# Kernel tuning notes

Measured on AMD Instinct MI355X. Metric: run time of the kernel, lower is better.

Reference implementation:

```python
import jax, jax.numpy as jnp
import numpy as np

# Whisper-small decoder, prefill path (text_offset == 0, no KV caches)
L, D, H, V, NCTX, S_AUDIO, B, T, MAXC = 12, 768, 12, 51865, 448, 1500, 2, 192, 256
DH = D // H
SCALE = DH ** -0.5
EPS = 1e-5

PNAMES = ['attn_ln_g', 'attn_ln_b', 'attn_q_w', 'attn_q_b', 'attn_k_w', 'attn_v_w', 'attn_v_b',
          'attn_o_w', 'attn_o_b', 'cross_ln_g', 'cross_ln_b', 'cross_q_w', 'cross_q_b',
          'cross_k_w', 'cross_v_w', 'cross_v_b', 'cross_o_w', 'cross_o_b',
          'mlp_ln_g', 'mlp_ln_b', 'mlp_w1', 'mlp_b1', 'mlp_w2', 'mlp_b2', 'ln_g', 'ln_b']


def _ln(x, g, b):
    m = jnp.mean(x, -1, keepdims=True)
    v = jnp.mean((x - m) ** 2, -1, keepdims=True)
    return (x - m) * jax.lax.rsqrt(v + EPS) * g + b


def _heads(t):
    b, t_, _ = t.shape
    return t.reshape(b, t_, H, DH).transpose(0, 2, 1, 3)  # (b,H,t,DH)


def _mha(q, k, v, mask):
    qh, kh, vh = _heads(q), _heads(k), _heads(v)
    qk = jnp.matmul(qh, kh.swapaxes(-1, -2)) * SCALE  # (B,H,Tq,Tk), broadcasts over kv batch 1
    if mask is not None:
        qk = qk + mask
    w = jax.nn.softmax(qk, axis=-1)
    o = jnp.matmul(w, vh)  # (B,H,Tq,DH)
    o = o.transpose(0, 2, 1, 3).reshape(q.shape[0], q.shape[1], D)
    return o, qk


def _lin(x, w, b=None):
    y = jnp.einsum('bti,oi->bto', x, w)
    return y if b is None else y + b


def _forward(x, xa, tok_emb, pos_emb, P):
    h = tok_emb[x] + pos_emb[:T]                        # (B,T,D)
    h = jnp.pad(h, ((0, 0), (0, MAXC - T), (0, 0)))     # pad to max_n_ctx_for_1st=256
    r = jnp.arange(MAXC)
    mask = jnp.where((r[None, :] > r[:, None]) | (r[None, :] >= T), -jnp.inf, 0.0)
    xa1 = xa[:1]                                        # xa.split(1)[0] in torch
    cross_qks, new_mkv, new_ckv = [], [], []
    for l in range(L):
        y = _ln(h, P['attn_ln_g'][l], P['attn_ln_b'][l])
        q = _lin(y, P['attn_q_w'][l], P['attn_q_b'][l])
        k = _lin(y, P['attn_k_w'][l])
        v = _lin(y, P['attn_v_w'][l], P['attn_v_b'][l])
        new_mkv += [k, v]
        o, _ = _mha(q, k, v, mask)
        h = h + _lin(o, P['attn_o_w'][l], P['attn_o_b'][l])
        y = _ln(h, P['cross_ln_g'][l], P['cross_ln_b'][l])
        q = _lin(y, P['cross_q_w'][l], P['cross_q_b'][l])
        ck = _lin(xa1, P['cross_k_w'][l])
        cv = _lin(xa1, P['cross_v_w'][l], P['cross_v_b'][l])
        new_ckv += [ck, cv]
        o, cqk = _mha(q, ck, cv, None)
        cross_qks.append(jax.lax.stop_gradient(cqk))    # qk.detach() in torch
        h = h + _lin(o, P['cross_o_w'][l], P['cross_o_b'][l])
        y = _ln(h, P['mlp_ln_g'][l], P['mlp_ln_b'][l])
        h = h + _lin(jax.nn.gelu(_lin(y, P['mlp_w1'][l], P['mlp_b1'][l]), approximate=False),
                     P['mlp_w2'][l], P['mlp_b2'][l])
    h = _ln(h, P['ln_g'], P['ln_b'])
    logits = jnp.matmul(h[:, :T], tok_emb.T).astype(jnp.float32)       # (B,T,V)
    cross_qks = jnp.concatenate(cross_qks, axis=0)[:, :, :T, :]        # (L*B,H,T,S_AUDIO)
    return logits, cross_qks, jnp.stack(new_mkv), jnp.stack(new_ckv)


def setup_inputs() -> dict:
    key = jax.random.key(0)
    ks = iter(jax.random.split(key, 48))
    def p(shape, s=0.02):
        return jax.random.normal(next(ks), shape, jnp.float32) * s
    inp = {
        'x': jax.random.randint(next(ks), (B, T), 0, V, dtype=jnp.int32),
        'xa': jax.random.normal(next(ks), (B, S_AUDIO, D), jnp.float32),
        'text_offset': 0,
        'isNewCKV': 1,
        'tok_emb': p((V, D)),
        'pos_emb': p((NCTX, D)),
        'attn_ln_g': 1.0 + p((L, D)), 'attn_ln_b': p((L, D)),
        'attn_q_w': p((L, D, D)), 'attn_q_b': p((L, D)),
        'attn_k_w': p((L, D, D)),
        'attn_v_w': p((L, D, D)), 'attn_v_b': p((L, D)),
        'attn_o_w': p((L, D, D)), 'attn_o_b': p((L, D)),
        'cross_ln_g': 1.0 + p((L, D)), 'cross_ln_b': p((L, D)),
        'cross_q_w': p((L, D, D)), 'cross_q_b': p((L, D)),
        'cross_k_w': p((L, D, D)),
        'cross_v_w': p((L, D, D)), 'cross_v_b': p((L, D)),
        'cross_o_w': p((L, D, D)), 'cross_o_b': p((L, D)),
        'mlp_ln_g': 1.0 + p((L, D)), 'mlp_ln_b': p((L, D)),
        'mlp_w1': p((L, 4 * D, D)), 'mlp_b1': p((L, 4 * D)),
        'mlp_w2': p((L, D, 4 * D)), 'mlp_b2': p((L, D)),
        'ln_g': 1.0 + p((D,)), 'ln_b': p((D,)),
    }
    return inp


def reference(x, xa, text_offset, isNewCKV, tok_emb, pos_emb,
              attn_ln_g, attn_ln_b, attn_q_w, attn_q_b, attn_k_w, attn_v_w, attn_v_b,
              attn_o_w, attn_o_b, cross_ln_g, cross_ln_b, cross_q_w, cross_q_b,
              cross_k_w, cross_v_w, cross_v_b, cross_o_w, cross_o_b,
              mlp_ln_g, mlp_ln_b, mlp_w1, mlp_b1, mlp_w2, mlp_b2, ln_g, ln_b):
    # text_offset == 0 prefill path; isNewCKV unused in the pure-python torch path
    P = dict(zip(PNAMES, (attn_ln_g, attn_ln_b, attn_q_w, attn_q_b, attn_k_w, attn_v_w, attn_v_b,
                          attn_o_w, attn_o_b, cross_ln_g, cross_ln_b, cross_q_w, cross_q_b,
                          cross_k_w, cross_v_w, cross_v_b, cross_o_w, cross_o_b,
                          mlp_ln_g, mlp_ln_b, mlp_w1, mlp_b1, mlp_w2, mlp_b2, ln_g, ln_b)))
    return _forward(x, xa, tok_emb, pos_emb, P)
```

## Files before the change

kernel.cpp:

```cpp
#include <hip/hip_runtime.h>
#include <math.h>

constexpr int kL = 12, kD = 768, kH = 12, kV = 51865, kSA = 1500;
constexpr int kB = 2, kT = 192, kMC = 256, kDH = 64;
constexpr float kScale = 0.125f;
constexpr float kEps = 1e-5f;
constexpr int kR = kB * kMC;
constexpr int kSLDc = 1504;

constexpr size_t SZ_LOGITS = (size_t)kB * kT * kV;
constexpr size_t SZ_CQK    = (size_t)kL * kB * kH * kT * kSA;
constexpr size_t SZ_MKV    = (size_t)2 * kL * kB * kMC * kD;
constexpr size_t OFF_CQK = SZ_LOGITS;
constexpr size_t OFF_MKV = OFF_CQK + SZ_CQK;
constexpr size_t OFF_CKV = OFF_MKV + SZ_MKV;

typedef float f32x4v __attribute__((ext_vector_type(4)));
typedef unsigned short us8v __attribute__((ext_vector_type(8)));
typedef unsigned short us4v __attribute__((ext_vector_type(4)));
typedef unsigned int   u32x4 __attribute__((ext_vector_type(4)));

static __device__ __forceinline__ unsigned short f2bf(float f) {
    unsigned int u = __float_as_uint(f);
    u += 0x7fffu + ((u >> 16) & 1u);
    return (unsigned short)(u >> 16);
}

static __device__ __forceinline__ unsigned int f2bf2(float lo, float hi) {
    unsigned int r;
    asm("v_cvt_pk_bf16_f32 %0, %1, %2" : "=v"(r) : "v"(lo), "v"(hi));
    return r;
}

static __device__ __forceinline__ float bf2f(unsigned short u) {
    return __uint_as_float((unsigned int)u << 16);
}

static __device__ __forceinline__ f32x4v mfma_bf16(us8v a, us8v b, f32x4v c) {
    asm("v_mfma_f32_16x16x32_bf16 %0, %1, %2, %0" : "+v"(c) : "v"(a), "v"(b));
    return c;
}

__global__ void k_embed(const int* __restrict__ x, const float* __restrict__ tok,
                        const float* __restrict__ pos, float* __restrict__ h)
{
    int idx = blockIdx.x * 256 + threadIdx.x;
    int d = idx % kD;
    int t = (idx / kD) % kMC;
    int b = idx / (kD * kMC);
    float v = 0.f;
    if (t < kT) {
        int tokid = x[b * kT + t];
        v = tok[(size_t)tokid * kD + d] + pos[(size_t)t * kD + d];
    }
    h[idx] = v;
}

__global__ void k_ln(const float* __restrict__ in, const float* __restrict__ g,
                     const float* __restrict__ bb, unsigned short* __restrict__ out)
{
    int r = blockIdx.x;
    const float* xr = in + (size_t)r * kD;
    int t = threadIdx.x;
    float x0 = xr[t], x1 = xr[t + 256], x2 = xr[t + 512];
    float s  = x0 + x1 + x2;
    float sq = x0 * x0 + x1 * x1 + x2 * x2;
    __shared__ float red[8];
    for (int o = 32; o > 0; o >>= 1) { s += __shfl_down(s, o); sq += __shfl_down(sq, o); }
    int w = t >> 6;
    if ((t & 63) == 0) { red[w] = s; red[4 + w] = sq; }
    __syncthreads();
    s  = red[0] + red[1] + red[2] + red[3];
    sq = red[4] + red[5] + red[6] + red[7];
    float m   = s * (1.f / kD);
    float var = sq * (1.f / kD) - m * m;
    float rs  = rsqrtf(var + kEps);
    unsigned short* orow = out + (size_t)r * kD;
    orow[t]       = f2bf((x0 - m) * rs * g[t]       + bb[t]);
    orow[t + 256] = f2bf((x1 - m) * rs * g[t + 256] + bb[t + 256]);
    orow[t + 512] = f2bf((x2 - m) * rs * g[t + 512] + bb[t + 512]);
}

__global__ void k_finalln(const float* __restrict__ h, const float* __restrict__ g,
                          const float* __restrict__ bb, unsigned short* __restrict__ out)
{
    int r = blockIdx.x;
    int b = r / kT, tt = r % kT;
    const float* xr = h + (size_t)(b * kMC + tt) * kD;
    int t = threadIdx.x;
    float x0 = xr[t], x1 = xr[t + 256], x2 = xr[t + 512];
    float s  = x0 + x1 + x2;
    float sq = x0 * x0 + x1 * x1 + x2 * x2;
    __shared__ float red[8];
    for (int o = 32; o > 0; o >>= 1) { s += __shfl_down(s, o); sq += __shfl_down(sq, o); }
    int w = t >> 6;
    if ((t & 63) == 0) { red[w] = s; red[4 + w] = sq; }
    __syncthreads();
    s  = red[0] + red[1] + red[2] + red[3];
    sq = red[4] + red[5] + red[6] + red[7];
    float m   = s * (1.f / kD);
    float var = sq * (1.f / kD) - m * m;
    float rs  = rsqrtf(var + kEps);
    unsigned short* orow = out + (size_t)r * kD;
    orow[t]       = f2bf((x0 - m) * rs * g[t]       + bb[t]);
    orow[t + 256] = f2bf((x1 - m) * rs * g[t + 256] + bb[t + 256]);
    orow[t + 512] = f2bf((x2 - m) * rs * g[t + 512] + bb[t + 512]);
}

struct GEntry { const float* W; const float* bias; const float* res; void* out; };
struct GBatch { GEntry e[24]; };

template <int ABF, int OBF>
__global__ __launch_bounds__(256)
void gemm_t(const void* __restrict__ Av, GBatch gb, int M, int N, int K,
            int dogelu)
{
    constexpr int LD = 72;
    __shared__ unsigned short As[3][64][LD];
    __shared__ unsigned short Ws[3][64][LD];
    const GEntry ge = gb.e[blockIdx.z];
    const float* __restrict__ W = ge.W;
    int bn = blockIdx.y * 64;
    int bm = blockIdx.x * 64;
    int tid = threadIdx.x;
    int wid = tid >> 6, lane = tid & 63;
    int wm = (wid >> 1) * 32, wn = (wid & 1) * 32;
    int l15 = lane & 15, lg = lane >> 4;
    int r = tid >> 2, cq = (tid & 3) * 16;
    int gr = bm + r, gc = bn + r;

    auto load_a = [&](int k0, u32x4& p0, u32x4& p1) {
        p0 = (u32x4){}; p1 = (u32x4){};
        if (ABF) {
            if (gr < M) {
                const unsigned short* ar =
                    (const unsigned short*)Av + (size_t)gr * K + k0 + cq;
                p0 = *(const u32x4*)ar;
                p1 = *(const u32x4*)(ar + 8);
            }
        } else {
            if (gr < M) {
                const float* ar = (const float*)Av + (size_t)gr * K + k0 + cq;
                float4 v0 = *(const float4*)(ar);
                float4 v1 = *(const float4*)(ar + 4);
                float4 v2 = *(const float4*)(ar + 8);
                float4 v3 = *(const float4*)(ar + 12);
                p0[0] = f2bf2(v0.x, v0.y); p0[1] = f2bf2(v0.z, v0.w);
                p0[2] = f2bf2(v1.x, v1.y); p0[3] = f2bf2(v1.z, v1.w);
                p1[0] = f2bf2(v2.x, v2.y); p1[1] = f2bf2(v2.z, v2.w);
                p1[2] = f2bf2(v3.x, v3.y); p1[3] = f2bf2(v3.z, v3.w);
            }
        }
    };
    auto load_w = [&](int k0, u32x4& p0, u32x4& p1) {
        p0 = (u32x4){}; p1 = (u32x4){};
        if (gc < N) {
            const float* wr = W + (size_t)gc * K + k0 + cq;
            float4 v0 = *(const float4*)(wr);
            float4 v1 = *(const float4*)(wr + 4);
            float4 v2 = *(const float4*)(wr + 8);
            float4 v3 = *(const float4*)(wr + 12);
            p0[0] = f2bf2(v0.x, v0.y); p0[1] = f2bf2(v0.z, v0.w);
            p0[2] = f2bf2(v1.x, v1.y); p0[3] = f2bf2(v1.z, v1.w);
            p1[0] = f2bf2(v2.x, v2.y); p1[1] = f2bf2(v2.z, v2.w);
            p1[2] = f2bf2(v3.x, v3.y); p1[3] = f2bf2(v3.z, v3.w);
        }
    };
    auto stage = [&](int buf, u32x4 a0, u32x4 a1, u32x4 w0, u32x4 w1) {
        *(u32x4*)&As[buf][r][cq]     = a0;
        *(u32x4*)&As[buf][r][cq + 8] = a1;
        *(u32x4*)&Ws[buf][r][cq]     = w0;
        *(u32x4*)&Ws[buf][r][cq + 8] = w1;
    };

    f32x4v acc00 = {}, acc01 = {}, acc10 = {}, acc11 = {};
    auto domfma = [&](int buf) {
        #pragma unroll
        for (int kc = 0; kc < 2; ++kc) {
            us8v af0 = *(const us8v*)&As[buf][wm + l15][kc * 32 + lg * 8];
            us8v af1 = *(const us8v*)&As[buf][wm + 16 + l15][kc * 32 + lg * 8];
            us8v wf0 = *(const us8v*)&Ws[buf][wn + l15][kc * 32 + lg * 8];
            us8v wf1 = *(const us8v*)&Ws[buf][wn + 16 + l15][kc * 32 + lg * 8];
            acc00 = mfma_bf16(af0, wf0, acc00);
            acc01 = mfma_bf16(af0, wf1, acc01);
            acc10 = mfma_bf16(af1, wf0, acc10);
            acc11 = mfma_bf16(af1, wf1, acc11);
        }
    };

    u32x4 a0A, a1A, w0A, w1A, a0B, a1B, w0B, w1B;
    load_a(0, a0A, a1A); load_w(0, w0A, w1A);
    stage(0, a0A, a1A, w0A, w1A);
    load_a(64, a0B, a1B); load_w(64, w0B, w1B);
    __syncthreads();

    int cur = 0;
    for (int k0 = 0; k0 < K; k0 += 128) {
        int n1 = cur + 1; if (n1 == 3) n1 = 0;
        int n2 = n1 + 1; if (n2 == 3) n2 = 0;
        if (k0 + 128 < K) { load_a(k0 + 128, a0A, a1A); load_w(k0 + 128, w0A, w1A); }
        domfma(cur);
        stage(n1, a0B, a1B, w0B, w1B);
        __syncthreads();
        if (k0 + 192 < K) { load_a(k0 + 192, a0B, a1B); load_w(k0 + 192, w0B, w1B); }
        domfma(n1);
        if (k0 + 128 < K) {
            stage(n2, a0A, a1A, w0A, w1A);
            __syncthreads();
        }
        cur = n2;
    }

    const float* bias = ge.bias;
    const float* res  = ge.res;
    f32x4v accs[2][2] = { { acc00, acc01 }, { acc10, acc11 } };
    #pragma unroll
    for (int fi = 0; fi < 2; ++fi) {
        #pragma unroll
        for (int fj = 0; fj < 2; ++fj) {
            int col = bn + wn + fj * 16 + l15;
            if (col >= N) continue;
            float bv = bias ? bias[col] : 0.f;
            #pragma unroll
            for (int rr = 0; rr < 4; ++rr) {
                int row = bm + wm + fi * 16 + lg * 4 + rr;
                if (row >= M) continue;
                float v = accs[fi][fj][rr] + bv;
                if (dogelu) v = 0.5f * v * (1.f + erff(v * 0.70710678118654752f));
                if (OBF) {
                    ((unsigned short*)ge.out)[(size_t)row * N + col] = f2bf(v);
                } else {
                    if (res) v += res[(size_t)row * N + col];
                    ((float*)ge.out)[(size_t)row * N + col] = v;
                }
            }
        }
    }
}

template <int OBF>
__global__ __launch_bounds__(256)
void gemm32(const unsigned short* __restrict__ A, GBatch gb, int M, int N, int K,
            int dogelu)
{
    constexpr int LD = 72;
    __shared__ unsigned short As[3][32][LD];
    __shared__ unsigned short Ws[3][64][LD];
    const GEntry ge = gb.e[blockIdx.z];
    const float* __restrict__ W = ge.W;
    int bn = blockIdx.y * 64;
    int bm = blockIdx.x * 32;
    int tid = threadIdx.x;
    int wid = tid >> 6, lane = tid & 63;
    int wr = (wid >> 1) * 16, wc = (wid & 1) * 32;
    int l15 = lane & 15, lg = lane >> 4;
    int ra = tid >> 3, ca = (tid & 7) * 8;
    int rw = tid >> 2, cw = (tid & 3) * 16;
    int gr = bm + ra, gc = bn + rw;

    auto load_a = [&](int k0, us8v& p) {
        p = (us8v){};
        if (gr < M) p = *(const us8v*)(A + (size_t)gr * K + k0 + ca);
    };
    auto load_w = [&](int k0, u32x4& p0, u32x4& p1) {
        p0 = (u32x4){}; p1 = (u32x4){};
        if (gc < N) {
            const float* wrp = W + (size_t)gc * K + k0 + cw;
            float4 v0 = *(const float4*)(wrp);
            float4 v1 = *(const float4*)(wrp + 4);
            float4 v2 = *(const float4*)(wrp + 8);
            float4 v3 = *(const float4*)(wrp + 12);
            p0[0] = f2bf2(v0.x, v0.y); p0[1] = f2bf2(v0.z, v0.w);
            p0[2] = f2bf2(v1.x, v1.y); p0[3] = f2bf2(v1.z, v1.w);
            p1[0] = f2bf2(v2.x, v2.y); p1[1] = f2bf2(v2.z, v2.w);
            p1[2] = f2bf2(v3.x, v3.y); p1[3] = f2bf2(v3.z, v3.w);
        }
    };
    auto stage = [&](int buf, us8v a, u32x4 w0, u32x4 w1) {
        *(us8v*)&As[buf][ra][ca]      = a;
        *(u32x4*)&Ws[buf][rw][cw]     = w0;
        *(u32x4*)&Ws[buf][rw][cw + 8] = w1;
    };

    f32x4v acc0 = {}, acc1 = {};
    auto domfma = [&](int buf) {
        #pragma unroll
        for (int kc = 0; kc < 2; ++kc) {
            us8v af  = *(const us8v*)&As[buf][wr + l15][kc * 32 + lg * 8];
            us8v wf0 = *(const us8v*)&Ws[buf][wc + l15][kc * 32 + lg * 8];
            us8v wf1 = *(const us8v*)&Ws[buf][wc + 16 + l15][kc * 32 + lg * 8];
            acc0 = mfma_bf16(af, wf0, acc0);
            acc1 = mfma_bf16(af, wf1, acc1);
        }
    };

    us8v aA, aB;
    u32x4 w0A, w1A, w0B, w1B;
    load_a(0, aA); load_w(0, w0A, w1A);
    stage(0, aA, w0A, w1A);
    load_a(64, aB); load_w(64, w0B, w1B);
    __syncthreads();

    int cur = 0;
    for (int k0 = 0; k0 < K; k0 += 128) {
        int n1 = cur + 1; if (n1 == 3) n1 = 0;
        int n2 = n1 + 1; if (n2 == 3) n2 = 0;
        if (k0 + 128 < K) { load_a(k0 + 128, aA); load_w(k0 + 128, w0A, w1A); }
        domfma(cur);
        stage(n1, aB, w0B, w1B);
        __syncthreads();
        if (k0 + 192 < K) { load_a(k0 + 192, aB); load_w(k0 + 192, w0B, w1B); }
        domfma(n1);
        if (k0 + 128 < K) {
            stage(n2, aA, w0A, w1A);
            __syncthreads();
        }
        cur = n2;
    }

    const float* bias = ge.bias;
    const float* res  = ge.res;
    f32x4v accs[2] = { acc0, acc1 };
    #pragma unroll
    for (int fj = 0; fj < 2; ++fj) {
        int col = bn + wc + fj * 16 + l15;
        if (col >= N) continue;
        float bv = bias ? bias[col] : 0.f;
        #pragma unroll
        for (int rr = 0; rr < 4; ++rr) {
            int row = bm + wr + lg * 4 + rr;
            if (row >= M) continue;
            float v = accs[fj][rr] + bv;
            if (dogelu) v = 0.5f * v * (1.f + erff(v * 0.70710678118654752f));
            if (OBF) {
                ((unsigned short*)ge.out)[(size_t)row * N + col] = f2bf(v);
            } else {
                if (res) v += res[(size_t)row * N + col];
                ((float*)ge.out)[(size_t)row * N + col] = v;
            }
        }
    }
}

__global__ __launch_bounds__(256)
void k_logits(const unsigned short* __restrict__ A, const float* __restrict__ W,
              float* __restrict__ out)
{
    constexpr int LD = 72;
    __shared__ unsigned short As[64][LD];
    __shared__ unsigned short Ws[2][64][LD];
    int bn = blockIdx.x * 64;
    int tid = threadIdx.x;
    int wid = tid >> 6, lane = tid & 63;
    int wm = (wid >> 1) * 32, wn = (wid & 1) * 32;
    int l15 = lane & 15, lg = lane >> 4;
    int r = tid >> 2, cq = (tid & 3) * 16;
    int gc = bn + r;

    auto load_w = [&](int k0, u32x4& p0, u32x4& p1) {
        p0 = (u32x4){}; p1 = (u32x4){};
        if (gc < kV) {
            const float* wr = W + (size_t)gc * kD + k0 + cq;
            float4 v0 = *(const float4*)(wr);
            float4 v1 = *(const float4*)(wr + 4);
            float4 v2 = *(const float4*)(wr + 8);
            float4 v3 = *(const float4*)(wr + 12);
            p0[0] = f2bf2(v0.x, v0.y); p0[1] = f2bf2(v0.z, v0.w);
            p0[2] = f2bf2(v1.x, v1.y); p0[3] = f2bf2(v1.z, v1.w);
            p1[0] = f2bf2(v2.x, v2.y); p1[1] = f2bf2(v2.z, v2.w);
            p1[2] = f2bf2(v3.x, v3.y); p1[3] = f2bf2(v3.z, v3.w);
        }
    };

    f32x4v acc[6][4];
    #pragma unroll
    for (int i = 0; i < 6; ++i)
        #pragma unroll
        for (int j = 0; j < 4; ++j) acc[i][j] = (f32x4v){};

    u32x4 rw0, rw1;
    load_w(0, rw0, rw1);
    *(u32x4*)&Ws[0][r][cq]     = rw0;
    *(u32x4*)&Ws[0][r][cq + 8] = rw1;
    __syncthreads();

    int cur = 0;
    for (int k0 = 0; k0 < kD; k0 += 64) {
        bool more = (k0 + 64) < kD;
        if (more) load_w(k0 + 64, rw0, rw1);
        #pragma unroll
        for (int mt = 0; mt < 6; ++mt) {
            {
                const unsigned short* ar = A + (size_t)(mt * 64 + r) * kD + k0 + cq;
                us8v v0 = *(const us8v*)ar;
                us8v v1 = *(const us8v*)(ar + 8);
                *(us8v*)&As[r][cq]     = v0;
                *(us8v*)&As[r][cq + 8] = v1;
            }
            __syncthreads();
            #pragma unroll
            for (int kc = 0; kc < 2; ++kc) {
                us8v af0 = *(const us8v*)&As[wm + l15][kc * 32 + lg * 8];
                us8v af1 = *(const us8v*)&As[wm + 16 + l15][kc * 32 + lg * 8];
                us8v wf0 = *(const us8v*)&Ws[cur][wn + l15][kc * 32 + lg * 8];
                us8v wf1 = *(const us8v*)&Ws[cur][wn + 16 + l15][kc * 32 + lg * 8];
                acc[mt][0] = mfma_bf16(af0, wf0, acc[mt][0]);
                acc[mt][1] = mfma_bf16(af0, wf1, acc[mt][1]);
                acc[mt][2] = mfma_bf16(af1, wf0, acc[mt][2]);
                acc[mt][3] = mfma_bf16(af1, wf1, acc[mt][3]);
            }
            __syncthreads();
        }
        if (more) {
            int nxt = cur ^ 1;
            *(u32x4*)&Ws[nxt][r][cq]     = rw0;
            *(u32x4*)&Ws[nxt][r][cq + 8] = rw1;
            cur = nxt;
        }
    }
    #pragma unroll
    for (int mt = 0; mt < 6; ++mt) {
        #pragma unroll
        for (int fi = 0; fi < 2; ++fi) {
            #pragma unroll
            for (int fj = 0; fj < 2; ++fj) {
                int col = bn + wn + fj * 16 + l15;
                if (col >= kV) continue;
                #pragma unroll
                for (int rr = 0; rr < 4; ++rr) {
                    int row = mt * 64 + wm + fi * 16 + lg * 4 + rr;
                    out[(size_t)row * kV + col] = acc[mt][fi * 2 + fj][rr];
                }
            }
        }
    }
}

template <int QBF>
__global__ __launch_bounds__(256)
void k_scores(const void* __restrict__ qv, const float* __restrict__ kk,
              unsigned short* __restrict__ sws, float* __restrict__ cqk,
              int Nk, int sld, int selfmask, int kPerB)
{
    constexpr int LD = 72;
    __shared__ unsigned short As[64][LD];
    __shared__ unsigned short Ks[64][LD];
    int z = blockIdx.z, b = z / kH, h = z % kH;
    int bm = blockIdx.x * 64, bn = blockIdx.y * 64;
    const float* kbase = kk + (kPerB ? (size_t)b * kMC * kD : 0) + (size_t)h * kDH;

    int tid = threadIdx.x;
    int r = tid >> 2, c0 = (tid & 3) * 16;
    {
        if (QBF) {
            const unsigned short* q = (const unsigned short*)qv;
            const unsigned short* qr =
                q + (size_t)(b * kMC + bm + r) * kD + h * kDH + c0;
            *(us8v*)&As[r][c0]     = *(const us8v*)qr;
            *(us8v*)&As[r][c0 + 8] = *(const us8v*)(qr + 8);
        } else {
            const float* q = (const float*)qv;
            const float* qr = q + (size_t)(b * kMC + bm + r) * kD + h * kDH + c0;
            float4 v0 = *(const float4*)(qr);
            float4 v1 = *(const float4*)(qr + 4);
            float4 v2 = *(const float4*)(qr + 8);
            float4 v3 = *(const float4*)(qr + 12);
            u32x4 p0, p1;
            p0[0] = f2bf2(v0.x, v0.y); p0[1] = f2bf2(v0.z, v0.w);
            p0[2] = f2bf2(v1.x, v1.y); p0[3] = f2bf2(v1.z, v1.w);
            p1[0] = f2bf2(v2.x, v2.y); p1[1] = f2bf2(v2.z, v2.w);
            p1[2] = f2bf2(v3.x, v3.y); p1[3] = f2bf2(v3.z, v3.w);
            *(u32x4*)&As[r][c0]     = p0;
            *(u32x4*)&As[r][c0 + 8] = p1;
        }
        int gk = bn + r;
        if (gk < Nk) {
            const float* kr = kbase + (size_t)gk * kD + c0;
            float4 v0 = *(const float4*)(kr);
            float4 v1 = *(const float4*)(kr + 4);
            float4 v2 = *(const float4*)(kr + 8);
            float4 v3 = *(const float4*)(kr + 12);
            u32x4 p0, p1;
            p0[0] = f2bf2(v0.x, v0.y); p0[1] = f2bf2(v0.z, v0.w);
            p0[2] = f2bf2(v1.x, v1.y); p0[3] = f2bf2(v1.z, v1.w);
            p1[0] = f2bf2(v2.x, v2.y); p1[1] = f2bf2(v2.z, v2.w);
            p1[2] = f2bf2(v3.x, v3.y); p1[3] = f2bf2(v3.z, v3.w);
            *(u32x4*)&Ks[r][c0]     = p0;
            *(u32x4*)&Ks[r][c0 + 8] = p1;
        } else {
            u32x4 zz = {};
            *(u32x4*)&Ks[r][c0]     = zz;
            *(u32x4*)&Ks[r][c0 + 8] = zz;
        }
    }
    __syncthreads();

    int wid = tid >> 6, lane = tid & 63;
    int wm = (wid >> 1) * 32, wn = (wid & 1) * 32;
    int l15 = lane & 15, lg = lane >> 4;

    f32x4v acc[2][2] = {};
    #pragma unroll
    for (int kc = 0; kc < 2; ++kc) {
        us8v a0 = *(const us8v*)&As[wm + l15][kc * 32 + lg * 8];
        us8v a1 = *(const us8v*)&As[wm + 16 + l15][kc * 32 + lg * 8];
        us8v b0 = *(const us8v*)&Ks[wn + l15][kc * 32 + lg * 8];
        us8v b1 = *(const us8v*)&Ks[wn + 16 + l15][kc * 32 + lg * 8];
        acc[0][0] = mfma_bf16(a0, b0, acc[0][0]);
        acc[0][1] = mfma_bf16(a0, b1, acc[0][1]);
        acc[1][0] = mfma_bf16(a1, b0, acc[1][0]);
        acc[1][1] = mfma_bf16(a1, b1, acc[1][1]);
    }

    #pragma unroll
    for (int fm = 0; fm < 2; ++fm) {
        #pragma unroll
        for (int fn = 0; fn < 2; ++fn) {
            int gj = bn + wn + fn * 16 + l15;
            if (gj >= Nk) continue;
            #pragma unroll
            for (int rr = 0; rr < 4; ++rr) {
                int gi = bm + wm + fm * 16 + lg * 4 + rr;
                float val = acc[fm][fn][rr] * kScale;
                if (cqk && gi < kT)
                    cqk[(((size_t)(b * kH + h)) * kT + gi) * kSA + gj] = val;
                if (selfmask && (gj > gi || gj >= kT)) val = -1e30f;
                sws[((size_t)z * kMC + gi) * sld + gj] = f2bf(val);
            }
        }
    }
}

constexpr int kCH  = 128;
constexpr int kLDK = 136;
__global__ __launch_bounds__(256)
void k_pv(const unsigned short* __restrict__ sws, const float* __restrict__ vv,
          unsigned short* __restrict__ o, int Nk, int sld, int vPerB)
{
    __shared__ unsigned short Pb[16][kLDK];
    __shared__ unsigned short Vt[64][kLDK];
    __shared__ float smx[16], sinv[16];
    int z = blockIdx.y, b = z / kH, h = z % kH;
    int i0 = blockIdx.x * 16;
    int t = threadIdx.x, wid = t >> 6, lane = t & 63;
    int l15 = lane & 15, lg = lane >> 4;
    const float* vbase = vv + (vPerB ? (size_t)b * kMC * kD : 0) + (size_t)h * kDH;

    for (int r2 = wid; r2 < 16; r2 += 4) {
        const unsigned short* srow2 = sws + ((size_t)z * kMC + i0 + r2) * sld;
        float mx = -3e38f;
        for (int j0 = lane * 8; j0 < Nk; j0 += 512) {
            us8v v = *(const us8v*)&srow2[j0];
            #pragma unroll
            for (int e = 0; e < 8; ++e)
                if (j0 + e < Nk) mx = fmaxf(mx, bf2f(v[e]));
        }
        for (int off = 32; off > 0; off >>= 1) mx = fmaxf(mx, __shfl_xor(mx, off));
        float sum = 0.f;
        for (int j0 = lane * 8; j0 < Nk; j0 += 512) {
            us8v v = *(const us8v*)&srow2[j0];
            #pragma unroll
            for (int e = 0; e < 8; ++e)
                if (j0 + e < Nk) sum += expf(bf2f(v[e]) - mx);
        }
        for (int off = 32; off > 0; off >>= 1) sum += __shfl_xor(sum, off);
        if (lane == 0) { smx[r2] = mx; sinv[r2] = 1.f / sum; }
    }
    __syncthreads();

    int pr = t >> 4;
    int jb = (t & 15) * 8;
    const unsigned short* srow = sws + ((size_t)z * kMC + i0 + pr) * sld;
    float mxv = smx[pr];

    f32x4v acc = {};
    for (int k0 = 0; k0 < Nk; k0 += kCH) {
        #pragma unroll
        for (int u = 0; u < 4; ++u) {
            int flat = t + u * 256;
            int kr = (flat >> 4) * 2;
            int c4 = flat & 15;
            float4 va = {0,0,0,0}, vb2 = {0,0,0,0};
            if (k0 + kr < Nk)
                va = *(const float4*)(vbase + (size_t)(k0 + kr) * kD + c4 * 4);
            if (k0 + kr + 1 < Nk)
                vb2 = *(const float4*)(vbase + (size_t)(k0 + kr + 1) * kD + c4 * 4);
            *(unsigned int*)&Vt[c4 * 4 + 0][kr] = f2bf2(va.x, vb2.x);
            *(unsigned int*)&Vt[c4 * 4 + 1][kr] = f2bf2(va.y, vb2.y);
            *(unsigned int*)&Vt[c4 * 4 + 2][kr] = f2bf2(va.z, vb2.z);
            *(unsigned int*)&Vt[c4 * 4 + 3][kr] = f2bf2(va.w, vb2.w);
        }
        {
            us8v praw = *(const us8v*)&srow[k0 + jb];
            #pragma unroll
            for (int u = 0; u < 8; u += 2) {
                int gj0 = k0 + jb + u;
                float e0 = (gj0     < Nk) ? expf(bf2f(praw[u])     - mxv) : 0.f;
                float e1 = (gj0 + 1 < Nk) ? expf(bf2f(praw[u + 1]) - mxv) : 0.f;
                *(unsigned int*)&Pb[pr][jb + u] = f2bf2(e0, e1);
            }
        }
        __syncthreads();
        #pragma unroll
        for (int kc = 0; kc < 4; ++kc) {
            us8v a  = *(const us8v*)&Pb[l15][kc * 32 + lg * 8];
            us8v bf = *(const us8v*)&Vt[wid * 16 + l15][kc * 32 + lg * 8];
            acc = mfma_bf16(a, bf, acc);
        }
        __syncthreads();
    }

    #pragma unroll
    for (int rr = 0; rr < 4; ++rr) {
        int row = lg * 4 + rr;
        float v = acc[rr] * sinv[row];
        o[(size_t)(b * kMC + i0 + row) * kD + h * kDH + wid * 16 + l15] = f2bf(v);
    }
}

extern "C" void kernel_launch(void* const* d_in, const int* in_sizes, int n_in,
                              void* d_out, int out_size, void* d_ws, size_t ws_size,
                              hipStream_t stream)
{
    const int*   x   = (const int*)  d_in[0];
    const float* xa  = (const float*)d_in[1];
    const float* tok = (const float*)d_in[4];
    const float* pos = (const float*)d_in[5];
    const float* attn_ln_g  = (const float*)d_in[6];
    const float* attn_ln_b  = (const float*)d_in[7];
    const float* attn_q_w   = (const float*)d_in[8];
    const float* attn_q_b   = (const float*)d_in[9];
    const float* attn_k_w   = (const float*)d_in[10];
    const float* attn_v_w   = (const float*)d_in[11];
    const float* attn_v_b   = (const float*)d_in[12];
    const float* attn_o_w   = (const float*)d_in[13];
    const float* attn_o_b   = (const float*)d_in[14];
    const float* cross_ln_g = (const float*)d_in[15];
    const float* cross_ln_b = (const float*)d_in[16];
    const float* cross_q_w  = (const float*)d_in[17];
    const float* cross_q_b  = (const float*)d_in[18];
    const float* cross_k_w  = (const float*)d_in[19];
    const float* cross_v_w  = (const float*)d_in[20];
    const float* cross_v_b  = (const float*)d_in[21];
    const float* cross_o_w  = (const float*)d_in[22];
    const float* cross_o_b  = (const float*)d_in[23];
    const float* mlp_ln_g   = (const float*)d_in[24];
    const float* mlp_ln_b   = (const float*)d_in[25];
    const float* mlp_w1     = (const float*)d_in[26];
    const float* mlp_b1     = (const float*)d_in[27];
    const float* mlp_w2     = (const float*)d_in[28];
    const float* mlp_b2     = (const float*)d_in[29];
    const float* ln_g       = (const float*)d_in[30];
    const float* ln_b       = (const float*)d_in[31];

    float* out = (float*)d_out;
    float* h    = (float*)d_ws;
    float* qws  = h   + (size_t)kR * kD;
    unsigned short* sS    = (unsigned short*)(qws + (size_t)kR * kD);
    unsigned short* y16   = sS   + (size_t)kB * kH * kMC * kSLDc;
    unsigned short* qb16  = y16  + (size_t)kR * kD;
    unsigned short* o16   = qb16 + (size_t)kR * kD;
    unsigned short* hid16 = o16  + (size_t)kR * kD;
    unsigned short* yF16  = hid16 + (size_t)kR * 4 * kD;

    k_embed<<<kB * kMC * kD / 256, 256, 0, stream>>>(x, tok, pos, h);

    {
        GBatch gc{};
        for (int l = 0; l < kL; ++l) {
            gc.e[2 * l]     = { cross_k_w + (size_t)l * kD * kD, nullptr, nullptr,
                                out + OFF_CKV + (size_t)(2 * l) * kSA * kD };
            gc.e[2 * l + 1] = { cross_v_w + (size_t)l * kD * kD, cross_v_b + (size_t)l * kD,
                                nullptr,
                                out + OFF_CKV + (size_t)(2 * l + 1) * kSA * kD };
        }
        gemm_t<0, 0><<<dim3((kSA + 63) / 64, kD / 64, 2 * kL), 256, 0, stream>>>(
            xa, gc, kSA, kD, kD, 0);
    }

    for (int l = 0; l < kL; ++l) {
        size_t dd = (size_t)l * kD * kD;
        float* kbuf  = out + OFF_MKV + (size_t)(2 * l)     * kB * kMC * kD;
        float* vbuf  = out + OFF_MKV + (size_t)(2 * l + 1) * kB * kMC * kD;
        float* ckbuf = out + OFF_CKV + (size_t)(2 * l)     * kSA * kD;
        float* cvbuf = out + OFF_CKV + (size_t)(2 * l + 1) * kSA * kD;
        float* cqk   = out + OFF_CQK + (size_t)l * kB * kH * kT * kSA;

        k_ln<<<kR, 256, 0, stream>>>(h, attn_ln_g + l * kD, attn_ln_b + l * kD, y16);
        {
            GBatch g3{};
            g3.e[0] = { attn_q_w + dd, attn_q_b + (size_t)l * kD, nullptr, qws };
            g3.e[1] = { attn_k_w + dd, nullptr,                   nullptr, kbuf };
            g3.e[2] = { attn_v_w + dd, attn_v_b + (size_t)l * kD, nullptr, vbuf };
            gemm32<0><<<dim3(kR / 32, kD / 64, 3), 256, 0, stream>>>(
                y16, g3, kR, kD, kD, 0);
        }
        k_scores<0><<<dim3(kMC / 64, kMC / 64, kB * kH), 256, 0, stream>>>(
            qws, kbuf, sS, nullptr, kMC, kMC, 1, 1);
        k_pv<<<dim3(kMC / 16, kB * kH), 256, 0, stream>>>(sS, vbuf, o16, kMC, kMC, 1);
        {
            GBatch g1{};
            g1.e[0] = { attn_o_w + dd, attn_o_b + (size_t)l * kD, h, h };
            gemm32<0><<<dim3(kR / 32, kD / 64, 1), 256, 0, stream>>>(
                o16, g1, kR, kD, kD, 0);
        }

        k_ln<<<kR, 256, 0, stream>>>(h, cross_ln_g + l * kD, cross_ln_b + l * kD, y16);
        {
            GBatch g1{};
            g1.e[0] = { cross_q_w + dd, cross_q_b + (size_t)l * kD, nullptr, qb16 };
            gemm32<1><<<dim3(kR / 32, kD / 64, 1), 256, 0, stream>>>(
                y16, g1, kR, kD, kD, 0);
        }
        k_scores<1><<<dim3(kMC / 64, (kSA + 63) / 64, kB * kH), 256, 0, stream>>>(
            qb16, ckbuf, sS, cqk, kSA, kSLDc, 0, 0);
        k_pv<<<dim3(kMC / 16, kB * kH), 256, 0, stream>>>(sS, cvbuf, o16, kSA, kSLDc, 0);
        {
            GBatch g1{};
            g1.e[0] = { cross_o_w + dd, cross_o_b + (size_t)l * kD, h, h };
            gemm32<0><<<dim3(kR / 32, kD / 64, 1), 256, 0, stream>>>(
                o16, g1, kR, kD, kD, 0);
        }

        k_ln<<<kR, 256, 0, stream>>>(h, mlp_ln_g + l * kD, mlp_ln_b + l * kD, y16);
        {
            GBatch g1{};
            g1.e[0] = { mlp_w1 + (size_t)l * 4 * kD * kD, mlp_b1 + (size_t)l * 4 * kD,
                        nullptr, hid16 };
            gemm32<1><<<dim3(kR / 32, 4 * kD / 64, 1), 256, 0, stream>>>(
                y16, g1, kR, 4 * kD, kD, 1);
        }
        {
            GBatch g1{};
            g1.e[0] = { mlp_w2 + (size_t)l * 4 * kD * kD, mlp_b2 + (size_t)l * kD, h, h };
            gemm32<0><<<dim3(kR / 32, kD / 64, 1), 256, 0, stream>>>(
                hid16, g1, kR, kD, 4 * kD, 0);
        }
    }

    k_finalln<<<kB * kT, 256, 0, stream>>>(h, ln_g, ln_b, yF16);
    k_logits<<<dim3((kV + 63) / 64), 256, 0, stream>>>(yF16, tok, out);
}
```

Before: 3.106 ms.

## Fuse LayerNorm into GEMM A-operand loading and drop separate LN kernels

Removes the three per-layer LayerNorm kernels and the bf16 y16 intermediate buffer. GEMMs consuming LN output now read fp32 h directly. Each block first computes per-row mean and rstd over its 32 rows, then normalizes, applies gamma/beta and converts to bf16 while loading A tiles. This saves 36 launches and a write/read round trip of the normalized activations. The cost is redundant row statistics and normalization in every column block, with twice the A-load bytes (fp32 instead of bf16), notably for the 48-column-block MLP1 GEMM.

```diff
diff --git a/kernel.cpp b/kernel.cpp
--- a/kernel.cpp
+++ b/kernel.cpp
@@ -54,31 +54,6 @@
         v = tok[(size_t)tokid * kD + d] + pos[(size_t)t * kD + d];
     }
     h[idx] = v;
-}
-
-__global__ void k_ln(const float* __restrict__ in, const float* __restrict__ g,
-                     const float* __restrict__ bb, unsigned short* __restrict__ out)
-{
-    int r = blockIdx.x;
-    const float* xr = in + (size_t)r * kD;
-    int t = threadIdx.x;
-    float x0 = xr[t], x1 = xr[t + 256], x2 = xr[t + 512];
-    float s  = x0 + x1 + x2;
-    float sq = x0 * x0 + x1 * x1 + x2 * x2;
-    __shared__ float red[8];
-    for (int o = 32; o > 0; o >>= 1) { s += __shfl_down(s, o); sq += __shfl_down(sq, o); }
-    int w = t >> 6;
-    if ((t & 63) == 0) { red[w] = s; red[4 + w] = sq; }
-    __syncthreads();
-    s  = red[0] + red[1] + red[2] + red[3];
-    sq = red[4] + red[5] + red[6] + red[7];
-    float m   = s * (1.f / kD);
-    float var = sq * (1.f / kD) - m * m;
-    float rs  = rsqrtf(var + kEps);
-    unsigned short* orow = out + (size_t)r * kD;
-    orow[t]       = f2bf((x0 - m) * rs * g[t]       + bb[t]);
-    orow[t + 256] = f2bf((x1 - m) * rs * g[t + 256] + bb[t + 256]);
-    orow[t + 512] = f2bf((x2 - m) * rs * g[t + 512] + bb[t + 512]);
 }
 
 __global__ void k_finalln(const float* __restrict__ h, const float* __restrict__ g,
@@ -238,14 +213,16 @@
     }
 }
 
-template <int OBF>
+template <int AMODE, int OBF>
 __global__ __launch_bounds__(256)
-void gemm32(const unsigned short* __restrict__ A, GBatch gb, int M, int N, int K,
-            int dogelu)
+void gemm32(const void* __restrict__ Av, GBatch gb, int M, int N, int K,
+            int dogelu, const float* __restrict__ lnG,
+            const float* __restrict__ lnB)
 {
     constexpr int LD = 72;
     __shared__ unsigned short As[3][32][LD];
     __shared__ unsigned short Ws[3][64][LD];
+    __shared__ float lnm[32], lnr[32];
     const GEntry ge = gb.e[blockIdx.z];
     const float* __restrict__ W = ge.W;
     int bn = blockIdx.y * 64;
@@ -258,9 +235,62 @@
     int rw = tid >> 2, cw = (tid & 3) * 16;
     int gr = bm + ra, gc = bn + rw;
 
+    float lnm_r = 0.f, lnr_r = 0.f;
+    if (AMODE == 1) {
+        int part = tid & 7;
+        float s = 0.f, sq = 0.f;
+        if (gr < M) {
+            const float* ar = (const float*)Av + (size_t)gr * K + part * 96;
+            #pragma unroll 8
+            for (int i = 0; i < 96; i += 4) {
+                float4 v = *(const float4*)(ar + i);
+                s  += v.x + v.y + v.z + v.w;
+                sq += v.x * v.x + v.y * v.y + v.z * v.z + v.w * v.w;
+            }
+        }
+        s += __shfl_xor(s, 1); sq += __shfl_xor(sq, 1);
+        s += __shfl_xor(s, 2); sq += __shfl_xor(sq, 2);
+        s += __shfl_xor(s, 4); sq += __shfl_xor(sq, 4);
+        if (part == 0) {
+            float m = s * (1.f / 768.f);
+            lnm[ra] = m;
+            lnr[ra] = rsqrtf(sq * (1.f / 768.f) - m * m + kEps);
+        }
+        __syncthreads();
+        lnm_r = lnm[ra];
+        lnr_r = lnr[ra];
+    }
+
     auto load_a = [&](int k0, us8v& p) {
         p = (us8v){};
-        if (gr < M) p = *(const us8v*)(A + (size_t)gr * K + k0 + ca);
+        if (gr < M) {
+            if (AMODE == 0) {
+                p = *(const us8v*)((const unsigned short*)Av +
+                                   (size_t)gr * K + k0 + ca);
+            } else {
+                const float* ar = (const float*)Av + (size_t)gr * K + k0 + ca;
+                float4 v0 = *(const float4*)(ar);
+                float4 v1 = *(const float4*)(ar + 4);
+                const float* gp = lnG + k0 + ca;
+                const float* bp = lnB + k0 + ca;
+                float4 g0 = *(const float4*)(gp);
+                float4 g1 = *(const float4*)(gp + 4);
+                float4 b0 = *(const float4*)(bp);
+                float4 b1 = *(const float4*)(bp + 4);
+                float a0 = (v0.x - lnm_r) * lnr_r * g0.x + b0.x;
+                float a1 = (v0.y - lnm_r) * lnr_r * g0.y + b0.y;
+                float a2 = (v0.z - lnm_r) * lnr_r * g0.z + b0.z;
+                float a3 = (v0.w - lnm_r) * lnr_r * g0.w + b0.w;
+                float a4 = (v1.x - lnm_r) * lnr_r * g1.x + b1.x;
+                float a5 = (v1.y - lnm_r) * lnr_r * g1.y + b1.y;
+                float a6 = (v1.z - lnm_r) * lnr_r * g1.z + b1.z;
+                float a7 = (v1.w - lnm_r) * lnr_r * g1.w + b1.w;
+                u32x4 q;
+                q[0] = f2bf2(a0, a1); q[1] = f2bf2(a2, a3);
+                q[2] = f2bf2(a4, a5); q[3] = f2bf2(a6, a7);
+                p = *(us8v*)&q;
+            }
+        }
     };
     auto load_w = [&](int k0, u32x4& p0, u32x4& p1) {
         p0 = (u32x4){}; p1 = (u32x4){};
@@ -657,8 +687,7 @@
     float* h    = (float*)d_ws;
     float* qws  = h   + (size_t)kR * kD;
     unsigned short* sS    = (unsigned short*)(qws + (size_t)kR * kD);
-    unsigned short* y16   = sS   + (size_t)kB * kH * kMC * kSLDc;
-    unsigned short* qb16  = y16  + (size_t)kR * kD;
+    unsigned short* qb16  = sS   + (size_t)kB * kH * kMC * kSLDc;
     unsigned short* o16   = qb16 + (size_t)kR * kD;
     unsigned short* hid16 = o16  + (size_t)kR * kD;
     unsigned short* yF16  = hid16 + (size_t)kR * 4 * kD;
@@ -686,14 +715,13 @@
         float* cvbuf = out + OFF_CKV + (size_t)(2 * l + 1) * kSA * kD;
         float* cqk   = out + OFF_CQK + (size_t)l * kB * kH * kT * kSA;
 
-        k_ln<<<kR, 256, 0, stream>>>(h, attn_ln_g + l * kD, attn_ln_b + l * kD, y16);
         {
             GBatch g3{};
             g3.e[0] = { attn_q_w + dd, attn_q_b + (size_t)l * kD, nullptr, qws };
             g3.e[1] = { attn_k_w + dd, nullptr,                   nullptr, kbuf };
             g3.e[2] = { attn_v_w + dd, attn_v_b + (size_t)l * kD, nullptr, vbuf };
-            gemm32<0><<<dim3(kR / 32, kD / 64, 3), 256, 0, stream>>>(
-                y16, g3, kR, kD, kD, 0);
+            gemm32<1, 0><<<dim3(kR / 32, kD / 64, 3), 256, 0, stream>>>(
+                h, g3, kR, kD, kD, 0, attn_ln_g + l * kD, attn_ln_b + l * kD);
         }
         k_scores<0><<<dim3(kMC / 64, kMC / 64, kB * kH), 256, 0, stream>>>(
             qws, kbuf, sS, nullptr, kMC, kMC, 1, 1);
@@ -701,16 +729,15 @@
         {
             GBatch g1{};
             g1.e[0] = { attn_o_w + dd, attn_o_b + (size_t)l * kD, h, h };
-            gemm32<0><<<dim3(kR / 32, kD / 64, 1), 256, 0, stream>>>(
-                o16, g1, kR, kD, kD, 0);
-        }
-
-        k_ln<<<kR, 256, 0, stream>>>(h, cross_ln_g + l * kD, cross_ln_b + l * kD, y16);
+            gemm32<0, 0><<<dim3(kR / 32, kD / 64, 1), 256, 0, stream>>>(
+                o16, g1, kR, kD, kD, 0, nullptr, nullptr);
+        }
+
         {
             GBatch g1{};
             g1.e[0] = { cross_q_w + dd, cross_q_b + (size_t)l * kD, nullptr, qb16 };
-            gemm32<1><<<dim3(kR / 32, kD / 64, 1), 256, 0, stream>>>(
-                y16, g1, kR, kD, kD, 0);
+            gemm32<1, 1><<<dim3(kR / 32, kD / 64, 1), 256, 0, stream>>>(
+                h, g1, kR, kD, kD, 0, cross_ln_g + l * kD, cross_ln_b + l * kD);
         }
         k_scores<1><<<dim3(kMC / 64, (kSA + 63) / 64, kB * kH), 256, 0, stream>>>(
             qb16, ckbuf, sS, cqk, kSA, kSLDc, 0, 0);
@@ -718,23 +745,22 @@
         {
             GBatch g1{};
             g1.e[0] = { cross_o_w + dd, cross_o_b + (size_t)l * kD, h, h };
-            gemm32<0><<<dim3(kR / 32, kD / 64, 1), 256, 0, stream>>>(
-                o16, g1, kR, kD, kD, 0);
-        }
-
-        k_ln<<<kR, 256, 0, stream>>>(h, mlp_ln_g + l * kD, mlp_ln_b + l * kD, y16);
+            gemm32<0, 0><<<dim3(kR / 32, kD / 64, 1), 256, 0, stream>>>(
+                o16, g1, kR, kD, kD, 0, nullptr, nullptr);
+        }
+
         {
             GBatch g1{};
             g1.e[0] = { mlp_w1 + (size_t)l * 4 * kD * kD, mlp_b1 + (size_t)l * 4 * kD,
                         nullptr, hid16 };
-            gemm32<1><<<dim3(kR / 32, 4 * kD / 64, 1), 256, 0, stream>>>(
-                y16, g1, kR, 4 * kD, kD, 1);
+            gemm32<1, 1><<<dim3(kR / 32, 4 * kD / 64, 1), 256, 0, stream>>>(
+                h, g1, kR, 4 * kD, kD, 1, mlp_ln_g + l * kD, mlp_ln_b + l * kD);
         }
         {
             GBatch g1{};
             g1.e[0] = { mlp_w2 + (size_t)l * 4 * kD * kD, mlp_b2 + (size_t)l * kD, h, h };
-            gemm32<0><<<dim3(kR / 32, kD / 64, 1), 256, 0, stream>>>(
-                hid16, g1, kR, kD, 4 * kD, 0);
+            gemm32<0, 0><<<dim3(kR / 32, kD / 64, 1), 256, 0, stream>>>(
+                hid16, g1, kR, kD, 4 * kD, 0, nullptr, nullptr);
         }
     }
 
```

Measured after the change: 3.396 ms. +9.3%, slower.

## Double-buffer A tiles in logits GEMM and pre-convert xa to bf16

Applied to the files above, without the earlier changes.

The logits kernel now double-buffers the A tile in shared memory and prefetches the next A (and W) tile into registers while MFMAs run on the current one. This cuts the number of barriers per iteration from two to one and hides global load latency. Separately, xa is converted to bf16 once, up front, so the 24-way batched cross K/V GEMM reads bf16 through the gemm_t<1,0> path instead of converting fp32 on every load. The extra conversion kernel and xa16 buffer add a little launch and workspace overhead.

```diff
diff --git a/kernel.cpp b/kernel.cpp
--- a/kernel.cpp
+++ b/kernel.cpp
@@ -54,6 +54,20 @@
         v = tok[(size_t)tokid * kD + d] + pos[(size_t)t * kD + d];
     }
     h[idx] = v;
+}
+
+__global__ void k_cvtbf(const float* __restrict__ in,
+                        unsigned short* __restrict__ out, int n8)
+{
+    int i = blockIdx.x * 256 + threadIdx.x;
+    if (i >= n8) return;
+    const float* p = in + (size_t)i * 8;
+    float4 v0 = *(const float4*)(p);
+    float4 v1 = *(const float4*)(p + 4);
+    u32x4 q;
+    q[0] = f2bf2(v0.x, v0.y); q[1] = f2bf2(v0.z, v0.w);
+    q[2] = f2bf2(v1.x, v1.y); q[3] = f2bf2(v1.z, v1.w);
+    *(u32x4*)&out[(size_t)i * 8] = q;
 }
 
 __global__ void k_ln(const float* __restrict__ in, const float* __restrict__ g,
@@ -347,7 +361,7 @@
               float* __restrict__ out)
 {
     constexpr int LD = 72;
-    __shared__ unsigned short As[64][LD];
+    __shared__ unsigned short As[2][64][LD];
     __shared__ unsigned short Ws[2][64][LD];
     int bn = blockIdx.x * 64;
     int tid = threadIdx.x;
@@ -371,6 +385,11 @@
             p1[2] = f2bf2(v3.x, v3.y); p1[3] = f2bf2(v3.z, v3.w);
         }
     };
+    auto load_a = [&](int k0, int mt, us8v& v0, us8v& v1) {
+        const unsigned short* ar = A + (size_t)(mt * 64 + r) * kD + k0 + cq;
+        v0 = *(const us8v*)ar;
+        v1 = *(const us8v*)(ar + 8);
+    };
 
     f32x4v acc[6][4];
     #pragma unroll
@@ -379,43 +398,49 @@
         for (int j = 0; j < 4; ++j) acc[i][j] = (f32x4v){};
 
     u32x4 rw0, rw1;
+    us8v ra0, ra1;
     load_w(0, rw0, rw1);
+    load_a(0, 0, ra0, ra1);
     *(u32x4*)&Ws[0][r][cq]     = rw0;
     *(u32x4*)&Ws[0][r][cq + 8] = rw1;
+    *(us8v*)&As[0][r][cq]      = ra0;
+    *(us8v*)&As[0][r][cq + 8]  = ra1;
     __syncthreads();
 
-    int cur = 0;
+    int acur = 0, wcur = 0;
     for (int k0 = 0; k0 < kD; k0 += 64) {
-        bool more = (k0 + 64) < kD;
-        if (more) load_w(k0 + 64, rw0, rw1);
+        bool morek = (k0 + 64) < kD;
+        if (morek) load_w(k0 + 64, rw0, rw1);
         #pragma unroll
         for (int mt = 0; mt < 6; ++mt) {
-            {
-                const unsigned short* ar = A + (size_t)(mt * 64 + r) * kD + k0 + cq;
-                us8v v0 = *(const us8v*)ar;
-                us8v v1 = *(const us8v*)(ar + 8);
-                *(us8v*)&As[r][cq]     = v0;
-                *(us8v*)&As[r][cq + 8] = v1;
-            }
-            __syncthreads();
+            bool last = !morek && (mt == 5);
+            if (!last) {
+                int nmt = (mt == 5) ? 0 : mt + 1;
+                int nk0 = (mt == 5) ? k0 + 64 : k0;
+                load_a(nk0, nmt, ra0, ra1);
+            }
             #pragma unroll
             for (int kc = 0; kc < 2; ++kc) {
-                us8v af0 = *(const us8v*)&As[wm + l15][kc * 32 + lg * 8];
-                us8v af1 = *(const us8v*)&As[wm + 16 + l15][kc * 32 + lg * 8];
-                us8v wf0 = *(const us8v*)&Ws[cur][wn + l15][kc * 32 + lg * 8];
-                us8v wf1 = *(const us8v*)&Ws[cur][wn + 16 + l15][kc * 32 + lg * 8];
+                us8v af0 = *(const us8v*)&As[acur][wm + l15][kc * 32 + lg * 8];
+                us8v af1 = *(const us8v*)&As[acur][wm + 16 + l15][kc * 32 + lg * 8];
+                us8v wf0 = *(const us8v*)&Ws[wcur][wn + l15][kc * 32 + lg * 8];
+                us8v wf1 = *(const us8v*)&Ws[wcur][wn + 16 + l15][kc * 32 + lg * 8];
                 acc[mt][0] = mfma_bf16(af0, wf0, acc[mt][0]);
                 acc[mt][1] = mfma_bf16(af0, wf1, acc[mt][1]);
                 acc[mt][2] = mfma_bf16(af1, wf0, acc[mt][2]);
                 acc[mt][3] = mfma_bf16(af1, wf1, acc[mt][3]);
             }
-            __syncthreads();
-        }
-        if (more) {
-            int nxt = cur ^ 1;
-            *(u32x4*)&Ws[nxt][r][cq]     = rw0;
-            *(u32x4*)&Ws[nxt][r][cq + 8] = rw1;
-            cur = nxt;
+            if (!last) {
+                *(us8v*)&As[acur ^ 1][r][cq]     = ra0;
+                *(us8v*)&As[acur ^ 1][r][cq + 8] = ra1;
+                if (mt == 5) {
+                    *(u32x4*)&Ws[wcur ^ 1][r][cq]     = rw0;
+                    *(u32x4*)&Ws[wcur ^ 1][r][cq + 8] = rw1;
+                }
+                __syncthreads();
+                acur ^= 1;
+                if (mt == 5) wcur ^= 1;
+            }
         }
     }
     #pragma unroll
@@ -662,8 +687,10 @@
     unsigned short* o16   = qb16 + (size_t)kR * kD;
     unsigned short* hid16 = o16  + (size_t)kR * kD;
     unsigned short* yF16  = hid16 + (size_t)kR * 4 * kD;
+    unsigned short* xa16  = yF16 + (size_t)kB * kT * kD;
 
     k_embed<<<kB * kMC * kD / 256, 256, 0, stream>>>(x, tok, pos, h);
+    k_cvtbf<<<(kSA * kD / 8 + 255) / 256, 256, 0, stream>>>(xa, xa16, kSA * kD / 8);
 
     {
         GBatch gc{};
@@ -674,8 +701,8 @@
                                 nullptr,
                                 out + OFF_CKV + (size_t)(2 * l + 1) * kSA * kD };
         }
-        gemm_t<0, 0><<<dim3((kSA + 63) / 64, kD / 64, 2 * kL), 256, 0, stream>>>(
-            xa, gc, kSA, kD, kD, 0);
+        gemm_t<1, 0><<<dim3((kSA + 63) / 64, kD / 64, 2 * kL), 256, 0, stream>>>(
+            xa16, gc, kSA, kD, kD, 0);
     }
 
     for (int l = 0; l < kL; ++l) {
```

New measurement: 3.064 ms. About the same (-1.4%).
